# Performance work log

Measured on AMD Instinct MI355X. Metric: run time of the kernel, lower is better.

## Reference

```python
import jax, jax.numpy as jnp
import numpy as np

N = 50000      # nodes
E = 800000     # edges (before self loops)
D = 128        # embedding_dimension
HEADS = 4
C = 32         # hidden_channels
NEG_SLOPE = 0.2


def setup_inputs() -> dict:
    key = jax.random.key(0)
    ks = jax.random.split(key, 12)
    s = 0.1
    x = jax.random.normal(ks[0], (N, D), jnp.float32)
    edge_index = jax.random.randint(ks[1], (2, E), 0, N)
    # layer 1: D -> HEADS*C, concat
    W1 = jax.random.normal(ks[2], (D, HEADS * C), jnp.float32) * s
    a_src1 = jax.random.normal(ks[3], (HEADS, C), jnp.float32) * s
    a_dst1 = jax.random.normal(ks[4], (HEADS, C), jnp.float32) * s
    b1 = jnp.zeros((HEADS * C,), jnp.float32)
    # layer 2: HEADS*C -> HEADS*C, concat
    W2 = jax.random.normal(ks[5], (HEADS * C, HEADS * C), jnp.float32) * s
    a_src2 = jax.random.normal(ks[6], (HEADS, C), jnp.float32) * s
    a_dst2 = jax.random.normal(ks[7], (HEADS, C), jnp.float32) * s
    b2 = jnp.zeros((HEADS * C,), jnp.float32)
    # layer 3: HEADS*C -> C, heads=1, no concat (mean over the single head)
    W3 = jax.random.normal(ks[8], (HEADS * C, C), jnp.float32) * s
    a_src3 = jax.random.normal(ks[9], (1, C), jnp.float32) * s
    a_dst3 = jax.random.normal(ks[10], (1, C), jnp.float32) * s
    b3 = jnp.zeros((C,), jnp.float32)
    return {"x": x, "edge_index": edge_index,
            "W1": W1, "a_src1": a_src1, "a_dst1": a_dst1, "b1": b1,
            "W2": W2, "a_src2": a_src2, "a_dst2": a_dst2, "b2": b2,
            "W3": W3, "a_src3": a_src3, "a_dst3": a_dst3, "b3": b3}


def gat_layer(x, src, dst, W, a_s, a_d, b, heads, concat):
    """One PyG-style GATConv (eval mode: dropout inactive).
    x: [N, Fin]; src/dst: [E2] (self loops included)."""
    n = x.shape[0]
    h = (x @ W).reshape(n, heads, -1)                 # [N, H, C]
    alpha_src = (h * a_s).sum(-1)                     # [N, H]
    alpha_dst = (h * a_d).sum(-1)                     # [N, H]
    logits = jax.nn.leaky_relu(alpha_src[src] + alpha_dst[dst], NEG_SLOPE)  # [E2, H]
    # segment softmax over destination nodes
    m = jax.ops.segment_max(logits, dst, num_segments=n)          # [N, H]
    ex = jnp.exp(logits - m[dst])                                  # [E2, H]
    denom = jax.ops.segment_sum(ex, dst, num_segments=n)          # [N, H]
    alpha = ex / (denom[dst] + 1e-16)                              # [E2, H]
    msg = h[src] * alpha[:, :, None]                               # [E2, H, C]
    out = jax.ops.segment_sum(msg, dst, num_segments=n)            # [N, H, C]
    if concat:
        return out.reshape(n, -1) + b
    return out.mean(axis=1) + b


def reference(x, edge_index, W1, a_src1, a_dst1, b1, W2, a_src2, a_dst2, b2,
              W3, a_src3, a_dst3, b3):
    loops = jnp.arange(N, dtype=edge_index.dtype)
    src = jnp.concatenate([edge_index[0], loops])   # add_self_loops=True
    dst = jnp.concatenate([edge_index[1], loops])
    h = gat_layer(x, src, dst, W1, a_src1, a_dst1, b1, HEADS, True)
    h = jax.nn.elu(h)
    h = gat_layer(h, src, dst, W2, a_src2, a_dst2, b2, HEADS, True)
    h = jax.nn.elu(h)
    out = gat_layer(h, src, dst, W3, a_src3, a_dst3, b3, 1, False)
    return out
```

## Files before the change

### kernel.cpp

```cpp
#include <hip/hip_runtime.h>
#include <cmath>

constexpr int NN  = 50000;
constexpr int EE  = 800000;
constexpr int E2C = EE + NN;

constexpr int NBUCK = 256;
constexpr int BW    = 196;
constexpr int EPT   = 8;
constexpr int CH    = 256 * EPT;
constexpr int NB_B  = (E2C + CH - 1) / CH;
constexpr int CAP   = 4096;
constexpr int SCAP  = 5120;
constexpr int G1ALL = (NN + 63) / 64;
constexpr int G1A   = 391;

using bf16x8 = __attribute__((ext_vector_type(8))) short;
using f32x4  = __attribute__((ext_vector_type(4))) float;

__device__ inline unsigned bf16rne(float f) {
    unsigned u = __builtin_bit_cast(unsigned, f);
    return (u + 0x7fffu + ((u >> 16) & 1u)) >> 16;
}
__device__ inline float bflo(unsigned u) { return __builtin_bit_cast(float, u << 16); }
__device__ inline float bfhi(unsigned u) { return __builtin_bit_cast(float, u & 0xffff0000u); }

__global__ __launch_bounds__(256) void cvt_weights(
    const float* __restrict__ W1, const float* __restrict__ W2,
    const float* __restrict__ W3,
    unsigned short* __restrict__ W1t, unsigned short* __restrict__ W2t,
    unsigned short* __restrict__ W3t, int* __restrict__ bcursor,
    float* __restrict__ AS1, float* __restrict__ AS2, float* __restrict__ AS3,
    unsigned short* __restrict__ H1, unsigned short* __restrict__ H2,
    unsigned short* __restrict__ H3)
{
    int g = blockIdx.x * 256 + threadIdx.x;
    if (g < NBUCK) bcursor[g] = 0;
    if (g < 4) { AS1[NN * 4 + g] = -1e30f; AS2[NN * 4 + g] = -1e30f; }
    if (g == 4) AS3[NN] = -1e30f;
    if (g < 128) { H1[(size_t)NN * 128 + g] = 0; H2[(size_t)NN * 128 + g] = 0; }
    if (g < 32)  H3[(size_t)NN * 32 + g] = 0;

    const float* W; unsigned short* Wt; int cols;
    if (g < 2048)      { W = W1; Wt = W1t; cols = 128; }
    else if (g < 4096) { W = W2; Wt = W2t; cols = 128; g -= 2048; }
    else if (g < 4608) { W = W3; Wt = W3t; cols = 32;  g -= 4096; }
    else return;
    int c  = g / 16;
    int k8 = (g % 16) * 8;
    unsigned up[4];
    #pragma unroll
    for (int j = 0; j < 4; ++j) {
        float a = W[(k8 + 2 * j) * cols + c];
        float b = W[(k8 + 2 * j + 1) * cols + c];
        up[j] = bf16rne(a) | (bf16rne(b) << 16);
    }
    uint4 u; u.x = up[0]; u.y = up[1]; u.z = up[2]; u.w = up[3];
    *(uint4*)(Wt + c * 128 + k8) = u;
}

template<int NT, int NH, bool F32IN>
__device__ inline void gemm_body(
    int bid, const void* __restrict__ inv, const unsigned short* __restrict__ Wt,
    const float* __restrict__ a_s, const float* __restrict__ a_d,
    unsigned short* __restrict__ hout, float* __restrict__ asrc,
    float* __restrict__ adst)
{
    constexpr int COLS = NT * 16;
    constexpr int TPH  = NT / NH;
    const int lane = threadIdx.x & 63;
    const int wave = threadIdx.x >> 6;
    const int m    = lane & 15;
    const int quad = lane >> 4;
    const int n0   = bid * 64 + wave * 16;

    int arow = n0 + m; if (arow >= NN) arow = NN - 1;

    f32x4 acc[NT] = {};
    #pragma unroll
    for (int kq = 0; kq < 4; ++kq) {
        bf16x8 a;
        if constexpr (F32IN) {
            const float* ap = (const float*)inv + (long long)arow * 128 + quad * 8 + kq * 32;
            float4 v0 = *(const float4*)ap;
            float4 v1 = *(const float4*)(ap + 4);
            a[0] = (short)bf16rne(v0.x); a[1] = (short)bf16rne(v0.y);
            a[2] = (short)bf16rne(v0.z); a[3] = (short)bf16rne(v0.w);
            a[4] = (short)bf16rne(v1.x); a[5] = (short)bf16rne(v1.y);
            a[6] = (short)bf16rne(v1.z); a[7] = (short)bf16rne(v1.w);
        } else {
            a = *(const bf16x8*)((const unsigned short*)inv
                    + (long long)arow * 128 + quad * 8 + kq * 32);
        }
        #pragma unroll
        for (int t = 0; t < NT; ++t) {
            bf16x8 b = *(const bf16x8*)(Wt + (t * 16 + m) * 128 + kq * 32 + quad * 8);
            acc[t] = __builtin_amdgcn_mfma_f32_16x16x32_bf16(a, b, acc[t], 0, 0, 0);
        }
    }

    #pragma unroll
    for (int r = 0; r < 4; ++r) {
        int node = n0 + quad * 4 + r;
        if (node < NN) {
            #pragma unroll
            for (int t = 0; t < NT; ++t)
                hout[(long long)node * COLS + t * 16 + m] =
                    (unsigned short)bf16rne(acc[t][r]);
        }
    }

    float asv[NT], adv[NT];
    #pragma unroll
    for (int t = 0; t < NT; ++t) { asv[t] = a_s[t * 16 + m]; adv[t] = a_d[t * 16 + m]; }

    #pragma unroll
    for (int r = 0; r < 4; ++r) {
        const int node = n0 + quad * 4 + r;
        #pragma unroll
        for (int hh = 0; hh < NH; ++hh) {
            float ps = 0.f, pd = 0.f;
            #pragma unroll
            for (int q = 0; q < TPH; ++q) {
                int t = hh * TPH + q;
                ps = fmaf(acc[t][r], asv[t], ps);
                pd = fmaf(acc[t][r], adv[t], pd);
            }
            #pragma unroll
            for (int off = 8; off > 0; off >>= 1) {
                ps += __shfl_down(ps, off, 16);
                pd += __shfl_down(pd, off, 16);
            }
            if (m == 0 && node < NN) {
                asrc[node * NH + hh] = ps;
                adst[node * NH + hh] = pd;
            }
        }
    }
}

__device__ inline void bin_body(
    int bid, const int* __restrict__ ei, int* __restrict__ bcursor,
    unsigned* __restrict__ pairs)
{
    __shared__ int cnt[NBUCK];
    __shared__ int scanex[NBUCK];
    __shared__ int base[NBUCK];
    __shared__ int cur[NBUCK];
    __shared__ unsigned stage[CH];

    const int tid = threadIdx.x;
    const long long e0 = (long long)bid * CH;
    cnt[tid] = 0;
    __syncthreads();

    unsigned rec[EPT]; int bk[EPT];
    #pragma unroll
    for (int j = 0; j < EPT; ++j) {
        long long e = e0 + tid + j * 256;
        bool valid = e < E2C;
        int ss = 0, dd = 0;
        if (valid) {
            if (e < EE) { ss = ei[e]; dd = ei[EE + e]; }
            else        { ss = dd = (int)(e - EE); }
        }
        int b = dd / BW;
        bk[j]  = valid ? b : -1;
        rec[j] = (unsigned)ss | ((unsigned)(dd - b * BW) << 16) | ((unsigned)b << 24);
        if (valid) atomicAdd(&cnt[b], 1);
    }
    __syncthreads();

    const int myc = cnt[tid];
    scanex[tid] = myc;
    __syncthreads();
    for (int off = 1; off < NBUCK; off <<= 1) {
        int t = (tid >= off) ? scanex[tid - off] : 0;
        __syncthreads();
        scanex[tid] += t;
        __syncthreads();
    }
    int excl = scanex[tid] - myc;
    __syncthreads();
    scanex[tid] = excl;
    cur[tid]    = excl;
    base[tid]   = atomicAdd(&bcursor[tid], myc);
    __syncthreads();

    #pragma unroll
    for (int j = 0; j < EPT; ++j) {
        if (bk[j] >= 0) {
            int p = atomicAdd(&cur[bk[j]], 1);
            stage[p] = rec[j];
        }
    }
    __syncthreads();

    const int total = (e0 + CH <= E2C) ? CH : (int)(E2C - e0);
    for (int j = tid; j < total; j += 256) {
        unsigned p = stage[j];
        int b = (int)(p >> 24);
        pairs[(size_t)b * CAP + base[b] + (j - scanex[b])] = p;
    }
}

__device__ inline void sort_body(
    int b, const int* __restrict__ bcursor, const unsigned* __restrict__ pairs,
    int2* __restrict__ rowp, unsigned short* __restrict__ sorted_src,
    unsigned short* __restrict__ perm)
{
    __shared__ int deg[256];
    __shared__ int scn[256];
    __shared__ int cur[256];
    __shared__ int hist2[64];
    __shared__ int scn2[64];
    __shared__ int cur2[64];
    const int n0 = b * BW;
    const int n1 = (n0 + BW < NN) ? n0 + BW : NN;
    const int nloc = n1 - n0;
    const int tid = threadIdx.x;
    const int mycnt = bcursor[b];
    const unsigned* seg = pairs + (size_t)b * CAP;
    const int base = b * SCAP;

    deg[tid] = 0;
    if (tid < 64) hist2[tid] = 0;
    __syncthreads();
    for (int i = tid; i < mycnt; i += 256)
        atomicAdd(&deg[(seg[i] >> 16) & 0xff], 1);
    __syncthreads();

    const int pv = (deg[tid] + 3) & ~3;
    int it = pv >> 2; if (it > 63) it = 63;
    scn[tid] = pv;
    if (tid < nloc) atomicAdd(&hist2[it], 1);
    __syncthreads();
    for (int off = 1; off < 256; off <<= 1) {
        int t = (tid >= off) ? scn[tid - off] : 0;
        __syncthreads();
        scn[tid] += t;
        __syncthreads();
    }
    if (tid < 64) scn2[tid] = hist2[tid];
    __syncthreads();
    for (int off = 1; off < 64; off <<= 1) {
        int t = (tid >= off && tid < 64) ? scn2[tid - off] : 0;
        __syncthreads();
        if (tid < 64) scn2[tid] += t;
        __syncthreads();
    }
    if (tid < 64) cur2[tid] = scn2[tid] - hist2[tid];
    __syncthreads();

    const int totalp = scn[255];
    const int pexcl  = scn[tid] - pv;
    cur[tid] = base + pexcl;
    if (tid < nloc) {
        int rank = atomicAdd(&cur2[it], 1);
        perm[n0 + rank] = (unsigned short)(n0 + tid);
        rowp[n0 + rank] = make_int2(base + pexcl, base + pexcl + pv);
    }
    __syncthreads();

    int lim = totalp + 8; if (lim > SCAP) lim = SCAP;
    for (int i = tid; i < lim; i += 256)
        sorted_src[base + i] = (unsigned short)NN;
    if (b == NBUCK - 1 && tid < 8)
        sorted_src[NBUCK * SCAP + tid] = (unsigned short)NN;
    __syncthreads();
    for (int i = tid; i < mycnt; i += 256) {
        unsigned p = seg[i];
        int pos = atomicAdd(&cur[(p >> 16) & 0xff], 1);
        sorted_src[pos] = (unsigned short)(p & 0xffff);
    }
}

__global__ __launch_bounds__(256) void bin_gemm(
    const int* __restrict__ ei, int* __restrict__ bcursor,
    unsigned* __restrict__ pairs,
    const float* __restrict__ x, const unsigned short* __restrict__ Wt,
    const float* __restrict__ a_s, const float* __restrict__ a_d,
    unsigned short* __restrict__ hout, float* __restrict__ asrc,
    float* __restrict__ adst)
{
    if (blockIdx.x < NB_B)
        bin_body(blockIdx.x, ei, bcursor, pairs);
    else
        gemm_body<8, 4, true>(blockIdx.x - NB_B, x, Wt, a_s, a_d, hout, asrc, adst);
}

__global__ __launch_bounds__(256) void sort_gemm(
    const int* __restrict__ bcursor, const unsigned* __restrict__ pairs,
    int2* __restrict__ rowp, unsigned short* __restrict__ sorted_src,
    unsigned short* __restrict__ perm,
    const float* __restrict__ x, const unsigned short* __restrict__ Wt,
    const float* __restrict__ a_s, const float* __restrict__ a_d,
    unsigned short* __restrict__ hout, float* __restrict__ asrc,
    float* __restrict__ adst)
{
    if (blockIdx.x < NBUCK)
        sort_body(blockIdx.x, bcursor, pairs, rowp, sorted_src, perm);
    else
        gemm_body<8, 4, true>(blockIdx.x - NBUCK + G1A, x, Wt, a_s, a_d,
                              hout, asrc, adst);
}

template<int COLS, int NH, bool DO_ELU>
__device__ inline void aggr_node(
    int d, int rk, int lc,
    const int2* __restrict__ rowp, const unsigned short* __restrict__ sorted_src,
    const unsigned short* __restrict__ hin,
    const float* __restrict__ asrc, const float* __restrict__ adst,
    const float* __restrict__ bias, float v[8])
{
    constexpr int USTR = COLS / 2;
    const int cc = lc * 8;
    const int head = cc / 32;
    const float ad = adst[d * NH + head];
    const int2 be = rowp[rk];
    const int beg = be.x, end = be.y;
    const uint* hp = (const uint*)hin + cc / 2;

    float num[8] = {};
    float den = 0.f;

    ushort4 sv = *(const ushort4*)&sorted_src[beg];
    for (int i = beg; i < end; i += 4) {
        ushort4 nx = *(const ushort4*)&sorted_src[i + 4];
        const int s[4] = {sv.x, sv.y, sv.z, sv.w};
        float a[4];
        uint4 Hv[4];
        #pragma unroll
        for (int j = 0; j < 4; ++j) a[j] = asrc[s[j] * NH + head];
        #pragma unroll
        for (int j = 0; j < 4; ++j)
            Hv[j] = *(const uint4*)&hp[(long long)s[j] * USTR];
        #pragma unroll
        for (int j = 0; j < 4; ++j) {
            float l = a[j] + ad; l = l > 0.f ? l : 0.2f * l;
            float w = __builtin_expf(l);
            den += w;
            num[0] = fmaf(w, bflo(Hv[j].x), num[0]); num[1] = fmaf(w, bfhi(Hv[j].x), num[1]);
            num[2] = fmaf(w, bflo(Hv[j].y), num[2]); num[3] = fmaf(w, bfhi(Hv[j].y), num[3]);
            num[4] = fmaf(w, bflo(Hv[j].z), num[4]); num[5] = fmaf(w, bfhi(Hv[j].z), num[5]);
            num[6] = fmaf(w, bflo(Hv[j].w), num[6]); num[7] = fmaf(w, bfhi(Hv[j].w), num[7]);
        }
        sv = nx;
    }

    float inv = 1.f / (den + 1e-16f);
    #pragma unroll
    for (int j = 0; j < 8; ++j) {
        v[j] = num[j] * inv + bias[cc + j];
        if (DO_ELU) v[j] = v[j] > 0.f ? v[j] : expm1f(v[j]);
    }
}

template<int NT_OUT, int NH_OUT>
__global__ __launch_bounds__(256) void aggr_gemm(
    const unsigned short* __restrict__ perm,
    const int2* __restrict__ rowp, const unsigned short* __restrict__ sorted_src,
    const unsigned short* __restrict__ hin,
    const float* __restrict__ asrc_in, const float* __restrict__ adst_in,
    const float* __restrict__ bias,
    const unsigned short* __restrict__ Wt,
    const float* __restrict__ a_s, const float* __restrict__ a_d,
    unsigned short* __restrict__ hout, float* __restrict__ asrc_out,
    float* __restrict__ adst_out)
{
    __shared__ unsigned short lds_h[16 * 128];
    __shared__ int lds_node[16];
    const int tid = threadIdx.x;
    const int row = tid / 16;
    const int lc  = tid % 16;
    const int rk  = blockIdx.x * 16 + row;
    const int d   = perm[rk];
    if (lc == 0) lds_node[row] = d;

    float v[8];
    aggr_node<128, 4, true>(d, rk, lc, rowp, sorted_src, hin, asrc_in, adst_in,
                            bias, v);

    uint4 u;
    u.x = bf16rne(v[0]) | (bf16rne(v[1]) << 16);
    u.y = bf16rne(v[2]) | (bf16rne(v[3]) << 16);
    u.z = bf16rne(v[4]) | (bf16rne(v[5]) << 16);
    u.w = bf16rne(v[6]) | (bf16rne(v[7]) << 16);
    *(uint4*)((char*)lds_h + row * 256 + ((lc * 16) ^ ((row & 7) << 4))) = u;
    __syncthreads();

    const int lane = tid & 63;
    const int wave = tid >> 6;
    const int m    = lane & 15;
    const int quad = lane >> 4;
    int t0;
    if constexpr (NT_OUT == 8) t0 = wave * 2;
    else { if (wave != 0) return; t0 = 0; }

    f32x4 acc[2] = {};
    #pragma unroll
    for (int kq = 0; kq < 4; ++kq) {
        int colb = (quad * 16 + kq * 64) ^ ((m & 7) << 4);
        bf16x8 a = *(const bf16x8*)((const char*)lds_h + m * 256 + colb);
        #pragma unroll
        for (int tt = 0; tt < 2; ++tt) {
            bf16x8 b = *(const bf16x8*)(Wt + ((t0 + tt) * 16 + m) * 128
                                        + kq * 32 + quad * 8);
            acc[tt] = __builtin_amdgcn_mfma_f32_16x16x32_bf16(a, b, acc[tt], 0, 0, 0);
        }
    }

    constexpr int COLS_OUT = NT_OUT * 16;
    const int head = t0 / (NT_OUT / NH_OUT);
    float asv[2], adv[2];
    #pragma unroll
    for (int tt = 0; tt < 2; ++tt) {
        asv[tt] = a_s[(t0 + tt) * 16 + m];
        adv[tt] = a_d[(t0 + tt) * 16 + m];
    }

    #pragma unroll
    for (int r = 0; r < 4; ++r) {
        const int node = lds_node[quad * 4 + r];
        #pragma unroll
        for (int tt = 0; tt < 2; ++tt)
            hout[(long long)node * COLS_OUT + (t0 + tt) * 16 + m] =
                (unsigned short)bf16rne(acc[tt][r]);
        float ps = acc[0][r] * asv[0];
        ps = fmaf(acc[1][r], asv[1], ps);
        float pd = acc[0][r] * adv[0];
        pd = fmaf(acc[1][r], adv[1], pd);
        #pragma unroll
        for (int off = 8; off > 0; off >>= 1) {
            ps += __shfl_down(ps, off, 16);
            pd += __shfl_down(pd, off, 16);
        }
        if (m == 0) {
            asrc_out[node * NH_OUT + head] = ps;
            adst_out[node * NH_OUT + head] = pd;
        }
    }
}

template<int COLS, int NH>
__global__ __launch_bounds__(256) void aggr_final(
    const unsigned short* __restrict__ perm,
    const int2* __restrict__ rowp, const unsigned short* __restrict__ sorted_src,
    const unsigned short* __restrict__ hin,
    const float* __restrict__ asrc, const float* __restrict__ adst,
    const float* __restrict__ bias, float* __restrict__ out)
{
    constexpr int TPN = COLS / 8;
    int t = blockIdx.x * 256 + threadIdx.x;
    int rk = t / TPN;
    int lc = t % TPN;
    if (rk >= NN) return;
    const int d = perm[rk];
    float v[8];
    aggr_node<COLS, NH, false>(d, rk, lc, rowp, sorted_src, hin, asrc, adst,
                               bias, v);
    float4 o0 = {v[0], v[1], v[2], v[3]};
    float4 o1 = {v[4], v[5], v[6], v[7]};
    *(float4*)&out[(long long)d * COLS + lc * 8]     = o0;
    *(float4*)&out[(long long)d * COLS + lc * 8 + 4] = o1;
}

extern "C" void kernel_launch(void* const* d_in, const int* in_sizes, int n_in,
                              void* d_out, int out_size, void* d_ws, size_t ws_size,
                              hipStream_t stream)
{
    const float* x   = (const float*)d_in[0];
    const int*   ei  = (const int*)  d_in[1];
    const float* W1  = (const float*)d_in[2];
    const float* as1 = (const float*)d_in[3];
    const float* ad1 = (const float*)d_in[4];
    const float* b1  = (const float*)d_in[5];
    const float* W2  = (const float*)d_in[6];
    const float* as2 = (const float*)d_in[7];
    const float* ad2 = (const float*)d_in[8];
    const float* b2  = (const float*)d_in[9];
    const float* W3  = (const float*)d_in[10];
    const float* as3 = (const float*)d_in[11];
    const float* ad3 = (const float*)d_in[12];
    const float* b3  = (const float*)d_in[13];
    float* out = (float*)d_out;

    unsigned short* H1  = (unsigned short*)d_ws;
    unsigned short* H2  = H1 + (size_t)(NN + 1) * 128;
    unsigned short* H3  = H2 + (size_t)(NN + 1) * 128;
    unsigned short* W1t = H3 + (size_t)(NN + 1) * 32;
    unsigned short* W2t = W1t + 128 * 128;
    unsigned short* W3t = W2t + 128 * 128;
    float* AS1 = (float*)(W3t + 32 * 128);
    float* AD1 = AS1 + (size_t)(NN + 1) * 4;
    float* AS2 = AD1 + (size_t)NN * 4;
    float* AD2 = AS2 + (size_t)(NN + 1) * 4;
    float* AS3 = AD2 + (size_t)NN * 4;
    float* AD3 = AS3 + (size_t)(NN + 1);
    int2* rowp = (int2*)(AD3 + NN);
    unsigned short* sorted = (unsigned short*)(rowp + NN);
    int* bcursor = (int*)(sorted + (size_t)NBUCK * SCAP + 8);
    unsigned short* perm = (unsigned short*)(bcursor + NBUCK);
    size_t off = ((size_t)(perm + NN) - (size_t)d_ws + 15) & ~(size_t)15;
    unsigned* pairs = (unsigned*)((char*)d_ws + off);

    const int gCvtW  = (4608 + 255) / 256;
    const int gBinG  = NB_B + G1A;
    const int gSortG = NBUCK + (G1ALL - G1A);
    const int gFused = NN / 16;
    const int gAggr3 = (NN * 4 + 255) / 256;

    cvt_weights<<<gCvtW, 256, 0, stream>>>(W1, W2, W3, W1t, W2t, W3t, bcursor,
                                           AS1, AS2, AS3, H1, H2, H3);
    bin_gemm<<<gBinG, 256, 0, stream>>>(ei, bcursor, pairs,
                                        x, W1t, as1, ad1, H1, AS1, AD1);
    sort_gemm<<<gSortG, 256, 0, stream>>>(bcursor, pairs, rowp, sorted, perm,
                                          x, W1t, as1, ad1, H1, AS1, AD1);
    aggr_gemm<8, 4><<<gFused, 256, 0, stream>>>(
        perm, rowp, sorted, H1, AS1, AD1, b1, W2t, as2, ad2, H2, AS2, AD2);
    aggr_gemm<2, 1><<<gFused, 256, 0, stream>>>(
        perm, rowp, sorted, H2, AS2, AD2, b2, W3t, as3, ad3, H3, AS3, AD3);
    aggr_final<32, 1><<<gAggr3, 256, 0, stream>>>(
        perm, rowp, sorted, H3, AS3, AD3, b3, out);
}
```

Baseline: 256.8 us.

## Split per-node edge aggregation across two thread halves and use raw exp2

The fused aggregate+GEMM kernels now launch 512 threads per block. Each node's edge list is split into two halves processed by separate thread groups, and the partial numerators and denominators are combined through LDS. The attention coefficients are pre-scaled by 1/ln2 so the inner loop can use the hardware v_exp_f32 (exp2) instruction instead of expf. The degree-bucket order in the sort is also reversed so high-degree nodes come first. These changes aim to cut the per-node serial edge-loop latency and the exp cost, in exchange for extra LDS traffic, an additional barrier and larger blocks.

```diff
diff --git a/kernel.cpp b/kernel.cpp
--- a/kernel.cpp
+++ b/kernel.cpp
@@ -14,6 +14,8 @@
 constexpr int SCAP  = 5120;
 constexpr int G1ALL = (NN + 63) / 64;
 constexpr int G1A   = 391;
+
+constexpr float RLN2 = 1.44269504088896340736f;
 
 using bf16x8 = __attribute__((ext_vector_type(8))) short;
 using f32x4  = __attribute__((ext_vector_type(4))) float;
@@ -112,7 +114,10 @@
 
     float asv[NT], adv[NT];
     #pragma unroll
-    for (int t = 0; t < NT; ++t) { asv[t] = a_s[t * 16 + m]; adv[t] = a_d[t * 16 + m]; }
+    for (int t = 0; t < NT; ++t) {
+        asv[t] = a_s[t * 16 + m] * RLN2;
+        adv[t] = a_d[t * 16 + m] * RLN2;
+    }
 
     #pragma unroll
     for (int r = 0; r < 4; ++r) {
@@ -232,6 +237,7 @@
 
     const int pv = (deg[tid] + 3) & ~3;
     int it = pv >> 2; if (it > 63) it = 63;
+    it = 63 - it;
     scn[tid] = pv;
     if (tid < nloc) atomicAdd(&hist2[it], 1);
     __syncthreads();
@@ -305,27 +311,17 @@
                               hout, asrc, adst);
 }
 
-template<int COLS, int NH, bool DO_ELU>
-__device__ inline void aggr_node(
-    int d, int rk, int lc,
-    const int2* __restrict__ rowp, const unsigned short* __restrict__ sorted_src,
-    const unsigned short* __restrict__ hin,
-    const float* __restrict__ asrc, const float* __restrict__ adst,
-    const float* __restrict__ bias, float v[8])
+template<int COLS, int NH>
+__device__ inline void aggr_range(
+    int b0, int e0, int head, float ad,
+    const unsigned short* __restrict__ sorted_src,
+    const uint* __restrict__ hp,
+    const float* __restrict__ asrc,
+    float num[8], float& den)
 {
     constexpr int USTR = COLS / 2;
-    const int cc = lc * 8;
-    const int head = cc / 32;
-    const float ad = adst[d * NH + head];
-    const int2 be = rowp[rk];
-    const int beg = be.x, end = be.y;
-    const uint* hp = (const uint*)hin + cc / 2;
-
-    float num[8] = {};
-    float den = 0.f;
-
-    ushort4 sv = *(const ushort4*)&sorted_src[beg];
-    for (int i = beg; i < end; i += 4) {
+    ushort4 sv = *(const ushort4*)&sorted_src[b0];
+    for (int i = b0; i < e0; i += 4) {
         ushort4 nx = *(const ushort4*)&sorted_src[i + 4];
         const int s[4] = {sv.x, sv.y, sv.z, sv.w};
         float a[4];
@@ -338,7 +334,8 @@
         #pragma unroll
         for (int j = 0; j < 4; ++j) {
             float l = a[j] + ad; l = l > 0.f ? l : 0.2f * l;
-            float w = __builtin_expf(l);
+            float w;
+            asm("v_exp_f32 %0, %1" : "=v"(w) : "v"(l));
             den += w;
             num[0] = fmaf(w, bflo(Hv[j].x), num[0]); num[1] = fmaf(w, bfhi(Hv[j].x), num[1]);
             num[2] = fmaf(w, bflo(Hv[j].y), num[2]); num[3] = fmaf(w, bfhi(Hv[j].y), num[3]);
@@ -347,17 +344,10 @@
         }
         sv = nx;
     }
-
-    float inv = 1.f / (den + 1e-16f);
-    #pragma unroll
-    for (int j = 0; j < 8; ++j) {
-        v[j] = num[j] * inv + bias[cc + j];
-        if (DO_ELU) v[j] = v[j] > 0.f ? v[j] : expm1f(v[j]);
-    }
 }
 
 template<int NT_OUT, int NH_OUT>
-__global__ __launch_bounds__(256) void aggr_gemm(
+__global__ __launch_bounds__(512) void aggr_gemm(
     const unsigned short* __restrict__ perm,
     const int2* __restrict__ rowp, const unsigned short* __restrict__ sorted_src,
     const unsigned short* __restrict__ hin,
@@ -370,27 +360,62 @@
 {
     __shared__ unsigned short lds_h[16 * 128];
     __shared__ int lds_node[16];
-    const int tid = threadIdx.x;
-    const int row = tid / 16;
-    const int lc  = tid % 16;
-    const int rk  = blockIdx.x * 16 + row;
-    const int d   = perm[rk];
-    if (lc == 0) lds_node[row] = d;
-
-    float v[8];
-    aggr_node<128, 4, true>(d, rk, lc, rowp, sorted_src, hin, asrc_in, adst_in,
-                            bias, v);
-
-    uint4 u;
-    u.x = bf16rne(v[0]) | (bf16rne(v[1]) << 16);
-    u.y = bf16rne(v[2]) | (bf16rne(v[3]) << 16);
-    u.z = bf16rne(v[4]) | (bf16rne(v[5]) << 16);
-    u.w = bf16rne(v[6]) | (bf16rne(v[7]) << 16);
-    *(uint4*)((char*)lds_h + row * 256 + ((lc * 16) ^ ((row & 7) << 4))) = u;
-    __syncthreads();
-
-    const int lane = tid & 63;
-    const int wave = tid >> 6;
+    __shared__ float lds_p[256][9];
+    const int tid   = threadIdx.x;
+    const int split = tid >> 8;
+    const int t8    = tid & 255;
+    const int row   = t8 >> 4;
+    const int lc    = t8 & 15;
+    const int rk    = blockIdx.x * 16 + row;
+    const int d     = perm[rk];
+    if (split == 0 && lc == 0) lds_node[row] = d;
+
+    const int cc   = lc * 8;
+    const int head = cc / 32;
+    const float ad = adst_in[d * 4 + head];
+    const uint* hp = (const uint*)hin + cc / 2;
+
+    const int2 be = rowp[rk];
+    const int beg = be.x, end = be.y;
+    const int half = (end - beg) >> 1;
+    const int mid  = beg + ((half + 3) & ~3);
+    const int b0 = split ? mid : beg;
+    const int e0 = split ? end : mid;
+
+    float num[8] = {};
+    float den = 0.f;
+    aggr_range<128, 4>(b0, e0, head, ad, sorted_src, hp, asrc_in, num, den);
+
+    if (split) {
+        #pragma unroll
+        for (int j = 0; j < 8; ++j) lds_p[t8][j] = num[j];
+        lds_p[t8][8] = den;
+    }
+    __syncthreads();
+
+    if (!split) {
+        #pragma unroll
+        for (int j = 0; j < 8; ++j) num[j] += lds_p[t8][j];
+        den += lds_p[t8][8];
+        float inv = 1.f / (den + 1e-16f);
+        float v[8];
+        #pragma unroll
+        for (int j = 0; j < 8; ++j) {
+            v[j] = num[j] * inv + bias[cc + j];
+            v[j] = v[j] > 0.f ? v[j] : expm1f(v[j]);
+        }
+        uint4 u;
+        u.x = bf16rne(v[0]) | (bf16rne(v[1]) << 16);
+        u.y = bf16rne(v[2]) | (bf16rne(v[3]) << 16);
+        u.z = bf16rne(v[4]) | (bf16rne(v[5]) << 16);
+        u.w = bf16rne(v[6]) | (bf16rne(v[7]) << 16);
+        *(uint4*)((char*)lds_h + row * 256 + ((lc * 16) ^ ((row & 7) << 4))) = u;
+    }
+    __syncthreads();
+    if (split) return;
+
+    const int lane = t8 & 63;
+    const int wave = t8 >> 6;
     const int m    = lane & 15;
     const int quad = lane >> 4;
     int t0;
@@ -411,12 +436,12 @@
     }
 
     constexpr int COLS_OUT = NT_OUT * 16;
-    const int head = t0 / (NT_OUT / NH_OUT);
+    const int headw = t0 / (NT_OUT / NH_OUT);
     float asv[2], adv[2];
     #pragma unroll
     for (int tt = 0; tt < 2; ++tt) {
-        asv[tt] = a_s[(t0 + tt) * 16 + m];
-        adv[tt] = a_d[(t0 + tt) * 16 + m];
+        asv[tt] = a_s[(t0 + tt) * 16 + m] * RLN2;
+        adv[tt] = a_d[(t0 + tt) * 16 + m] * RLN2;
     }
 
     #pragma unroll
@@ -436,8 +461,8 @@
             pd += __shfl_down(pd, off, 16);
         }
         if (m == 0) {
-            asrc_out[node * NH_OUT + head] = ps;
-            adst_out[node * NH_OUT + head] = pd;
+            asrc_out[node * NH_OUT + headw] = ps;
+            adst_out[node * NH_OUT + headw] = pd;
         }
     }
 }
@@ -456,9 +481,18 @@
     int lc = t % TPN;
     if (rk >= NN) return;
     const int d = perm[rk];
+    const int cc = lc * 8;
+    const int head = cc / 32;
+    const float ad = adst[d * NH + head];
+    const int2 be = rowp[rk];
+    const uint* hp = (const uint*)hin + cc / 2;
+    float num[8] = {};
+    float den = 0.f;
+    aggr_range<COLS, NH>(be.x, be.y, head, ad, sorted_src, hp, asrc, num, den);
+    float inv = 1.f / (den + 1e-16f);
     float v[8];
-    aggr_node<COLS, NH, false>(d, rk, lc, rowp, sorted_src, hin, asrc, adst,
-                               bias, v);
+    #pragma unroll
+    for (int j = 0; j < 8; ++j) v[j] = num[j] * inv + bias[cc + j];
     float4 o0 = {v[0], v[1], v[2], v[3]};
     float4 o1 = {v[4], v[5], v[6], v[7]};
     *(float4*)&out[(long long)d * COLS + lc * 8]     = o0;
@@ -516,9 +550,9 @@
                                         x, W1t, as1, ad1, H1, AS1, AD1);
     sort_gemm<<<gSortG, 256, 0, stream>>>(bcursor, pairs, rowp, sorted, perm,
                                           x, W1t, as1, ad1, H1, AS1, AD1);
-    aggr_gemm<8, 4><<<gFused, 256, 0, stream>>>(
+    aggr_gemm<8, 4><<<gFused, 512, 0, stream>>>(
         perm, rowp, sorted, H1, AS1, AD1, b1, W2t, as2, ad2, H2, AS2, AD2);
-    aggr_gemm<2, 1><<<gFused, 256, 0, stream>>>(
+    aggr_gemm<2, 1><<<gFused, 512, 0, stream>>>(
         perm, rowp, sorted, H2, AS2, AD2, b2, W3t, as3, ad3, H3, AS3, AD3);
     aggr_final<32, 1><<<gAggr3, 256, 0, stream>>>(
         perm, rowp, sorted, H3, AS3, AD3, b3, out);
```

Result: no change. 253.5 us, median of 2 (-1.3%).
